# Kernel tuning notes

Measured on AMD Instinct MI355X. Metric: run time of the kernel, lower is better.

## Reference

```python
import jax, jax.numpy as jnp
import numpy as np

# --- geometry constants (ProtoDUNE-HD-like) ---
B, F, T = 1, 1, 256            # batch, input features, nticks
NCHANS = 2560                   # total readout channels (800+800+480+480)
NWIRES = [800, 800, 480]        # wires per plane (U, V, W) on each face
NCELLS = 40000                  # number of 3-wire crossing cells per face
MLP_HID, MLP_OUT = 8, 2

# channel ranges per (face, plane): induction planes (U,V) wrap both faces,
# collection (W) channels are disjoint per face
_CHAN_RANGES = {(0, 0): (0, 800), (0, 1): (800, 1600), (0, 2): (1600, 2080),
                (1, 0): (0, 800), (1, 1): (800, 1600), (1, 2): (2080, 2560)}


def _make_tables():
    rng = np.random.default_rng(0)
    wcs = {}
    for (f, p), (lo, hi) in _CHAN_RANGES.items():
        n = hi - lo
        ch = lo + rng.permutation(n)                       # irregular wire->channel map
        wcs[(f, p)] = np.stack([np.arange(n), ch], axis=1).astype(np.int64)
    gi = {}
    for f in (0, 1):
        gi[f] = np.stack([rng.integers(0, NWIRES[p], NCELLS) for p in range(3)],
                         axis=1).astype(np.int64)          # (NCELLS, 3) wire idx per plane
    return wcs, gi


def setup_inputs() -> dict:
    key = jax.random.key(0)
    k = jax.random.split(key, 5)
    wcs, gi = _make_tables()
    inp = {
        'x':  jax.random.normal(k[0], (B, F, NCHANS, T), jnp.float32),
        'W1': jax.random.normal(k[1], (3 * F, MLP_HID), jnp.float32) * 0.5,
        'b1': jax.random.normal(k[2], (MLP_HID,), jnp.float32) * 0.1,
        'W2': jax.random.normal(k[3], (MLP_HID, MLP_OUT), jnp.float32) * 0.5,
        'b2': jax.random.normal(k[4], (MLP_OUT,), jnp.float32) * 0.1,
        'gi0': jnp.asarray(gi[0]), 'gi1': jnp.asarray(gi[1]),
    }
    for f in (0, 1):
        for p in range(3):
            inp[f'wc{f}{p}'] = jnp.asarray(wcs[(f, p)])
    return inp


def _make_wires(x, wc):
    # wires[..., wire_ident, :] = x[..., channel, :]   (Network.make_wires)
    Bb, Ff, _, Tt = x.shape
    wires = jnp.zeros((Bb, Ff, wc.shape[0], Tt), x.dtype)
    return wires.at[:, :, wc[:, 0], :].set(x[:, :, wc[:, 1], :])


def _crossview_mlp(x, W1, b1, W2, b2, wcs, gis):
    # mp_step: relu -> per-face cross-view gather -> MLP -> amax scatter -> concat
    x = jax.nn.relu(x)
    Bb, Ff, C, Tt = x.shape
    scattered = jnp.zeros((Bb, MLP_OUT, C, Tt), x.dtype)   # zeros init => amax includes 0
    for f in range(2):
        gi = gis[f]
        # gather the three plane views for each crossing cell: (B, 3F, NCELLS, T)
        cells = jnp.concatenate(
            [_make_wires(x, wcs[f][p])[:, :, gi[:, p], :] for p in range(3)], axis=1)
        h = jnp.einsum('bfnt,fh->bhnt', cells, W1) + b1[None, :, None, None]
        y = jnp.einsum('bhnt,ho->bont', h, W2) + b2[None, :, None, None]
        # scatter_to_chans: amax-reduce cell outputs back onto readout channels
        for p in range(3):
            ch = wcs[f][p][gi[:, p], 1]                    # channel of each cell's wire
            scattered = scattered.at[:, :, ch, :].max(y)
    # special_style == 'mlp': concat input features with cross-view MLP features
    return jnp.concatenate([x, scattered], axis=1)         # (B, F+MLP_OUT, C, T)


def reference(x, W1, b1, W2, b2, wc00, wc01, wc02, wc10, wc11, wc12, gi0, gi1):
    wcs = ((wc00, wc01, wc02), (wc10, wc11, wc12))
    gis = (gi0, gi1)
    return _crossview_mlp(x, W1, b1, W2, b2, wcs, gis)
```

## Files before the change

kernel.cpp:

```cpp
#include <hip/hip_runtime.h>
#include <hip/hip_fp16.h>

#define NCHANS 2560
#define TT 256
#define NCELLS_ 40000
#define NINST 240000
#define HALF_NINST 120000
#define CAP 192

#define WS_CURSOR 0
#define WS_XR     16384
#define WS_EPACK  1327104

#define PREP_BLOCKS 640
#define FILL_BLOCKS 938

__device__ __forceinline__ __half2 pk_max_f16(__half2 a, __half2 b) {
    unsigned int ua = *(unsigned int*)&a;
    unsigned int ub = *(unsigned int*)&b;
    unsigned int ur;
    asm("v_pk_max_f16 %0, %1, %2" : "=v"(ur) : "v"(ua), "v"(ub));
    return *(__half2*)&ur;
}

__global__ __launch_bounds__(256) void zero_cursor_kernel(int* __restrict__ cursor) {
    const int i = blockIdx.x * 256 + threadIdx.x;
    cursor[i] = 0;
}

__global__ __launch_bounds__(256) void prep_fill_kernel(
    const float* __restrict__ x,
    const int* __restrict__ gi0, const int* __restrict__ gi1,
    const int* __restrict__ wc00, const int* __restrict__ wc01, const int* __restrict__ wc02,
    const int* __restrict__ wc10, const int* __restrict__ wc11, const int* __restrict__ wc12,
    int* __restrict__ cursor, uint2* __restrict__ epack, uint2* __restrict__ xr,
    float* __restrict__ out)
{
    const int b = blockIdx.x;
    if (b < PREP_BLOCKS) {
        const int i = b * 256 + threadIdx.x;
        float4 v = ((const float4*)x)[i];
        v.x = fmaxf(v.x, 0.f); v.y = fmaxf(v.y, 0.f);
        v.z = fmaxf(v.z, 0.f); v.w = fmaxf(v.w, 0.f);
        ((float4*)out)[i] = v;
        __half2 h01 = __floats2half2_rn(v.x, v.y);
        __half2 h23 = __floats2half2_rn(v.z, v.w);
        uint2 p;
        p.x = *(unsigned int*)&h01;
        p.y = *(unsigned int*)&h23;
        xr[i] = p;
    } else {
        const int j = (b - PREP_BLOCKS) * 256 + threadIdx.x;
        if (j >= NINST) return;
        const int face = (j >= HALF_NINST) ? 1 : 0;
        const int i = j - face * HALF_NINST;
        const int p = i % 3;
        const int cellBase = i - p;
        const int* gi = face ? gi1 : gi0;
        const int w0 = gi[cellBase + 0];
        const int w1 = gi[cellBase + 1];
        const int w2 = gi[cellBase + 2];
        const int* wcA = face ? wc10 : wc00;
        const int* wcB = face ? wc11 : wc01;
        const int* wcC = face ? wc12 : wc02;
        const int c0 = wcA[w0 * 2 + 1];
        const int c1 = wcB[w1 * 2 + 1];
        const int c2 = wcC[w2 * 2 + 1];
        const int cOwn = (p == 0) ? c0 : ((p == 1) ? c1 : c2);
        uint2 E;
        E.x = (unsigned)c0 | ((unsigned)c1 << 16);
        E.y = (unsigned)c2;
        const int s = atomicAdd(&cursor[cOwn], 1);
        if (s < CAP) epack[cOwn * CAP + s] = E;
    }
}

__global__ __launch_bounds__(256) void gather_kernel(
    const float* __restrict__ W1, const float* __restrict__ b1,
    const float* __restrict__ W2, const float* __restrict__ b2,
    const int* __restrict__ cursor, const uint2* __restrict__ epack,
    const char* __restrict__ xr, float* __restrict__ out)
{
    float A[3][2], C[2];
#pragma unroll
    for (int o = 0; o < 2; ++o) {
        float s = b2[o];
#pragma unroll
        for (int h = 0; h < 8; ++h) s += b1[h] * W2[h * 2 + o];
        C[o] = s;
    }
#pragma unroll
    for (int p = 0; p < 3; ++p)
#pragma unroll
        for (int o = 0; o < 2; ++o) {
            float s = 0.f;
#pragma unroll
            for (int h = 0; h < 8; ++h) s += W1[p * 8 + h] * W2[h * 2 + o];
            A[p][o] = s;
        }
    __half2 a2[3][2], C2[2];
#pragma unroll
    for (int p = 0; p < 3; ++p)
#pragma unroll
        for (int o = 0; o < 2; ++o) a2[p][o] = __half2half2(__float2half(A[p][o]));
    C2[0] = __half2half2(__float2half(C[0]));
    C2[1] = __half2half2(__float2half(C[1]));

    const int w = threadIdx.x >> 6;
    const int lane = threadIdx.x & 63;
    const int wid = blockIdx.x * 4 + w;
    int ch = wid >> 1;
    const int half = wid & 1;
    ch = __builtin_amdgcn_readfirstlane(ch);

    int n = cursor[ch];
    n = n < CAP ? n : CAP;
    const uint2* ep = epack + ch * CAP;
    const char* base = xr + half * 256 + lane * 4;

    __half2 m0 = __half2half2(__float2half(0.f));
    __half2 m1 = m0;

#pragma unroll 2
    for (int e = 0; e < n; ++e) {
        const uint2 E = ep[e];
        const int c0 = E.x & 0xFFFFu;
        const int c1 = E.x >> 16;
        const int c2 = E.y;
        const __half2 f0 = *(const __half2*)(base + (c0 << 9));
        const __half2 f1 = *(const __half2*)(base + (c1 << 9));
        const __half2 f2 = *(const __half2*)(base + (c2 << 9));
        const __half2 y0 = __hfma2(a2[0][0], f0, __hfma2(a2[1][0], f1, __hfma2(a2[2][0], f2, C2[0])));
        const __half2 y1 = __hfma2(a2[0][1], f0, __hfma2(a2[1][1], f1, __hfma2(a2[2][1], f2, C2[1])));
        m0 = pk_max_f16(m0, y0);
        m1 = pk_max_f16(m1, y1);
    }

    const int off = ch * TT + half * 128 + lane * 2;
    float2* o1 = (float2*)(out + NCHANS * TT + off);
    float2* o2 = (float2*)(out + 2 * NCHANS * TT + off);
    *o1 = make_float2(__low2float(m0), __high2float(m0));
    *o2 = make_float2(__low2float(m1), __high2float(m1));
}

extern "C" void kernel_launch(void* const* d_in, const int* in_sizes, int n_in,
                              void* d_out, int out_size, void* d_ws, size_t ws_size,
                              hipStream_t stream) {
    const float* x  = (const float*)d_in[0];
    const float* W1 = (const float*)d_in[1];
    const float* b1 = (const float*)d_in[2];
    const float* W2 = (const float*)d_in[3];
    const float* b2 = (const float*)d_in[4];
    const int* gi0  = (const int*)d_in[5];
    const int* gi1  = (const int*)d_in[6];
    const int* wc00 = (const int*)d_in[7];
    const int* wc01 = (const int*)d_in[8];
    const int* wc02 = (const int*)d_in[9];
    const int* wc10 = (const int*)d_in[10];
    const int* wc11 = (const int*)d_in[11];
    const int* wc12 = (const int*)d_in[12];
    float* out = (float*)d_out;

    char* ws = (char*)d_ws;
    int*   cursor = (int*)(ws + WS_CURSOR);
    uint2* xr     = (uint2*)(ws + WS_XR);
    uint2* epack  = (uint2*)(ws + WS_EPACK);

    zero_cursor_kernel<<<NCHANS / 256, 256, 0, stream>>>(cursor);

    prep_fill_kernel<<<PREP_BLOCKS + FILL_BLOCKS, 256, 0, stream>>>(
        x, gi0, gi1, wc00, wc01, wc02, wc10, wc11, wc12,
        cursor, epack, xr, out);

    gather_kernel<<<NCHANS * 2 / 4, 256, 0, stream>>>(
        W1, b1, W2, b2, cursor, epack, (const char*)xr, out);
}
```

Baseline: 76.00 us.

## Hoist own-channel term, split entry list across waves, stage entries in LDS

Each bucket entry now stores only the two other channels, since the owning channel's contribution is the same for every entry. That term is precomputed once per channel as a base value, which cuts per-entry gathers from three to two and halves entry size. Each wave now covers the full time row with 8-byte loads, and the entry list is split in half across two waves, with the partial maxima merged through shared memory and a block barrier. Entries are staged in LDS before the loop. The cost is a sync plus extra shared memory in exchange for fewer global loads per entry.

```diff
diff --git a/kernel.cpp b/kernel.cpp
--- a/kernel.cpp
+++ b/kernel.cpp
@@ -3,10 +3,10 @@
 
 #define NCHANS 2560
 #define TT 256
-#define NCELLS_ 40000
 #define NINST 240000
 #define HALF_NINST 120000
 #define CAP 192
+#define HRANGE 96
 
 #define WS_CURSOR 0
 #define WS_XR     16384
@@ -22,10 +22,11 @@
     asm("v_pk_max_f16 %0, %1, %2" : "=v"(ur) : "v"(ua), "v"(ub));
     return *(__half2*)&ur;
 }
+__device__ __forceinline__ __half2 u2h(unsigned int u) { return *(__half2*)&u; }
+__device__ __forceinline__ unsigned int h2u(__half2 h) { return *(unsigned int*)&h; }
 
 __global__ __launch_bounds__(256) void zero_cursor_kernel(int* __restrict__ cursor) {
-    const int i = blockIdx.x * 256 + threadIdx.x;
-    cursor[i] = 0;
+    cursor[blockIdx.x * 256 + threadIdx.x] = 0;
 }
 
 __global__ __launch_bounds__(256) void prep_fill_kernel(
@@ -33,7 +34,7 @@
     const int* __restrict__ gi0, const int* __restrict__ gi1,
     const int* __restrict__ wc00, const int* __restrict__ wc01, const int* __restrict__ wc02,
     const int* __restrict__ wc10, const int* __restrict__ wc11, const int* __restrict__ wc12,
-    int* __restrict__ cursor, uint2* __restrict__ epack, uint2* __restrict__ xr,
+    int* __restrict__ cursor, unsigned int* __restrict__ epack, uint2* __restrict__ xr,
     float* __restrict__ out)
 {
     const int b = blockIdx.x;
@@ -46,8 +47,8 @@
         __half2 h01 = __floats2half2_rn(v.x, v.y);
         __half2 h23 = __floats2half2_rn(v.z, v.w);
         uint2 p;
-        p.x = *(unsigned int*)&h01;
-        p.y = *(unsigned int*)&h23;
+        p.x = h2u(h01);
+        p.y = h2u(h23);
         xr[i] = p;
     } else {
         const int j = (b - PREP_BLOCKS) * 256 + threadIdx.x;
@@ -67,9 +68,9 @@
         const int c1 = wcB[w1 * 2 + 1];
         const int c2 = wcC[w2 * 2 + 1];
         const int cOwn = (p == 0) ? c0 : ((p == 1) ? c1 : c2);
-        uint2 E;
-        E.x = (unsigned)c0 | ((unsigned)c1 << 16);
-        E.y = (unsigned)c2;
+        const int cA   = (p == 0) ? c1 : c0;
+        const int cB   = (p == 2) ? c1 : c2;
+        const unsigned int E = (unsigned)cA | ((unsigned)cB << 16);
         const int s = atomicAdd(&cursor[cOwn], 1);
         if (s < CAP) epack[cOwn * CAP + s] = E;
     }
@@ -78,16 +79,16 @@
 __global__ __launch_bounds__(256) void gather_kernel(
     const float* __restrict__ W1, const float* __restrict__ b1,
     const float* __restrict__ W2, const float* __restrict__ b2,
-    const int* __restrict__ cursor, const uint2* __restrict__ epack,
-    const char* __restrict__ xr, float* __restrict__ out)
+    const int* __restrict__ cursor, const unsigned int* __restrict__ epack,
+    const uint2* __restrict__ xr, float* __restrict__ out)
 {
-    float A[3][2], C[2];
+    float Af[3][2], Cf[2];
 #pragma unroll
     for (int o = 0; o < 2; ++o) {
         float s = b2[o];
 #pragma unroll
         for (int h = 0; h < 8; ++h) s += b1[h] * W2[h * 2 + o];
-        C[o] = s;
+        Cf[o] = s;
     }
 #pragma unroll
     for (int p = 0; p < 3; ++p)
@@ -96,51 +97,79 @@
             float s = 0.f;
 #pragma unroll
             for (int h = 0; h < 8; ++h) s += W1[p * 8 + h] * W2[h * 2 + o];
-            A[p][o] = s;
+            Af[p][o] = s;
         }
     __half2 a2[3][2], C2[2];
 #pragma unroll
     for (int p = 0; p < 3; ++p)
 #pragma unroll
-        for (int o = 0; o < 2; ++o) a2[p][o] = __half2half2(__float2half(A[p][o]));
-    C2[0] = __half2half2(__float2half(C[0]));
-    C2[1] = __half2half2(__float2half(C[1]));
+        for (int o = 0; o < 2; ++o) a2[p][o] = __half2half2(__float2half(Af[p][o]));
+    C2[0] = __half2half2(__float2half(Cf[0]));
+    C2[1] = __half2half2(__float2half(Cf[1]));
+
+    __shared__ unsigned int sEnt[4][HRANGE];
+    __shared__ uint4 sM[2][64];
 
     const int w = threadIdx.x >> 6;
     const int lane = threadIdx.x & 63;
-    const int wid = blockIdx.x * 4 + w;
-    int ch = wid >> 1;
-    const int half = wid & 1;
+    const int slot = w >> 1;
+    const int halfIdx = w & 1;
+    int ch = blockIdx.x * 2 + slot;
     ch = __builtin_amdgcn_readfirstlane(ch);
+
+    const int p = (ch >= 1600) ? 2 : ((ch >= 800) ? 1 : 0);
+    const int pA = (p == 0) ? 1 : 0;
+    const int pB = (p == 2) ? 1 : 2;
+    const __half2 aA0 = a2[pA][0], aB0 = a2[pB][0];
+    const __half2 aA1 = a2[pA][1], aB1 = a2[pB][1];
 
     int n = cursor[ch];
     n = n < CAP ? n : CAP;
-    const uint2* ep = epack + ch * CAP;
-    const char* base = xr + half * 256 + lane * 4;
-
-    __half2 m0 = __half2half2(__float2half(0.f));
-    __half2 m1 = m0;
-
-#pragma unroll 2
-    for (int e = 0; e < n; ++e) {
-        const uint2 E = ep[e];
-        const int c0 = E.x & 0xFFFFu;
-        const int c1 = E.x >> 16;
-        const int c2 = E.y;
-        const __half2 f0 = *(const __half2*)(base + (c0 << 9));
-        const __half2 f1 = *(const __half2*)(base + (c1 << 9));
-        const __half2 f2 = *(const __half2*)(base + (c2 << 9));
-        const __half2 y0 = __hfma2(a2[0][0], f0, __hfma2(a2[1][0], f1, __hfma2(a2[2][0], f2, C2[0])));
-        const __half2 y1 = __hfma2(a2[0][1], f0, __hfma2(a2[1][1], f1, __hfma2(a2[2][1], f2, C2[1])));
-        m0 = pk_max_f16(m0, y0);
-        m1 = pk_max_f16(m1, y1);
-    }
-
-    const int off = ch * TT + half * 128 + lane * 2;
-    float2* o1 = (float2*)(out + NCHANS * TT + off);
-    float2* o2 = (float2*)(out + 2 * NCHANS * TT + off);
-    *o1 = make_float2(__low2float(m0), __high2float(m0));
-    *o2 = make_float2(__low2float(m1), __high2float(m1));
+    const int lo = halfIdx ? (n >> 1) : 0;
+    const int hi = halfIdx ? n : (n >> 1);
+    const int cnt = hi - lo;
+
+    for (int e0 = lane; e0 < cnt; e0 += 64)
+        sEnt[w][e0] = epack[ch * CAP + lo + e0];
+
+    const uint2 dOwn = xr[ch * 64 + lane];
+    const __half2 base00 = __hfma2(a2[p][0], u2h(dOwn.x), C2[0]);
+    const __half2 base01 = __hfma2(a2[p][0], u2h(dOwn.y), C2[0]);
+    const __half2 base10 = __hfma2(a2[p][1], u2h(dOwn.x), C2[1]);
+    const __half2 base11 = __hfma2(a2[p][1], u2h(dOwn.y), C2[1]);
+
+    __half2 m00 = __half2half2(__float2half(0.f));
+    __half2 m01 = m00, m10 = m00, m11 = m00;
+
+#pragma unroll 4
+    for (int e = 0; e < cnt; ++e) {
+        const unsigned int E = sEnt[w][e];
+        const int cA = E & 0xFFFFu;
+        const int cB = E >> 16;
+        const uint2 dA = xr[cA * 64 + lane];
+        const uint2 dB = xr[cB * 64 + lane];
+        const __half2 y00 = __hfma2(aA0, u2h(dA.x), __hfma2(aB0, u2h(dB.x), base00));
+        const __half2 y01 = __hfma2(aA0, u2h(dA.y), __hfma2(aB0, u2h(dB.y), base01));
+        const __half2 y10 = __hfma2(aA1, u2h(dA.x), __hfma2(aB1, u2h(dB.x), base10));
+        const __half2 y11 = __hfma2(aA1, u2h(dA.y), __hfma2(aB1, u2h(dB.y), base11));
+        m00 = pk_max_f16(m00, y00); m01 = pk_max_f16(m01, y01);
+        m10 = pk_max_f16(m10, y10); m11 = pk_max_f16(m11, y11);
+    }
+
+    if (halfIdx) sM[slot][lane] = make_uint4(h2u(m00), h2u(m01), h2u(m10), h2u(m11));
+    __syncthreads();
+    if (!halfIdx) {
+        const uint4 o = sM[slot][lane];
+        m00 = pk_max_f16(m00, u2h(o.x));
+        m01 = pk_max_f16(m01, u2h(o.y));
+        m10 = pk_max_f16(m10, u2h(o.z));
+        m11 = pk_max_f16(m11, u2h(o.w));
+        const int off = ch * TT + lane * 4;
+        *(float4*)(out + NCHANS * TT + off) =
+            make_float4(__low2float(m00), __high2float(m00), __low2float(m01), __high2float(m01));
+        *(float4*)(out + 2 * NCHANS * TT + off) =
+            make_float4(__low2float(m10), __high2float(m10), __low2float(m11), __high2float(m11));
+    }
 }
 
 extern "C" void kernel_launch(void* const* d_in, const int* in_sizes, int n_in,
@@ -162,9 +191,9 @@
     float* out = (float*)d_out;
 
     char* ws = (char*)d_ws;
-    int*   cursor = (int*)(ws + WS_CURSOR);
-    uint2* xr     = (uint2*)(ws + WS_XR);
-    uint2* epack  = (uint2*)(ws + WS_EPACK);
+    int*          cursor = (int*)(ws + WS_CURSOR);
+    uint2*        xr     = (uint2*)(ws + WS_XR);
+    unsigned int* epack  = (unsigned int*)(ws + WS_EPACK);
 
     zero_cursor_kernel<<<NCHANS / 256, 256, 0, stream>>>(cursor);
 
@@ -172,6 +201,6 @@
         x, gi0, gi1, wc00, wc01, wc02, wc10, wc11, wc12,
         cursor, epack, xr, out);
 
-    gather_kernel<<<NCHANS * 2 / 4, 256, 0, stream>>>(
-        W1, b1, W2, b2, cursor, epack, (const char*)xr, out);
-}
+    gather_kernel<<<NCHANS / 2, 256, 0, stream>>>(
+        W1, b1, W2, b2, cursor, epack, xr, out);
+}
```

Result: no change. 76.50 us (+0.7%).
